# Kernel optimization log

Measured on AMD Instinct MI355X. Metric: run time of the kernel, lower is better.

## Reference

```python
import jax, jax.numpy as jnp
import numpy as np


def setup_inputs() -> dict:
    key = jax.random.key(0)
    k1, k2 = jax.random.split(key)
    B, C, H, W = 8, 16, 512, 512
    x = jax.random.normal(k1, (B, C, H, W), dtype=jnp.float32)
    # displacement field in voxel units, channels-first like the torch module
    phi = jax.random.normal(k2, (B, 2, H, W), dtype=jnp.float32) * 3.0
    return {"x": x, "phi": phi}


def _pull2d_wrap(img, disp):
    """img: [B,H,W,C], disp: [B,H,W,2] (displacement in voxels).
    Linear interpolation with circulant ('dft') boundary = wrap via mod."""
    B, H, W, C = img.shape
    gy = jnp.arange(H, dtype=img.dtype)[:, None]   # [H,1]
    gx = jnp.arange(W, dtype=img.dtype)[None, :]   # [1,W]
    cy = disp[..., 0] + gy                          # [B,H,W] sample coords (abs)
    cx = disp[..., 1] + gx
    y0f = jnp.floor(cy)
    x0f = jnp.floor(cx)
    wy = (cy - y0f)[..., None]                      # [B,H,W,1]
    wx = (cx - x0f)[..., None]
    y0 = jnp.mod(y0f.astype(jnp.int32), H)
    x0 = jnp.mod(x0f.astype(jnp.int32), W)
    y1 = jnp.mod(y0 + 1, H)
    x1 = jnp.mod(x0 + 1, W)

    def gather(im, yi, xi):                         # im [H,W,C]; yi,xi [H,W]
        return im[yi, xi]

    g = jax.vmap(gather)
    v00 = g(img, y0, x0)
    v01 = g(img, y0, x1)
    v10 = g(img, y1, x0)
    v11 = g(img, y1, x1)
    top = v00 * (1 - wx) + v01 * wx
    bot = v10 * (1 - wx) + v11 * wx
    return top * (1 - wy) + bot * wy                # [B,H,W,C]


def reference(x, phi):
    # x: [B,C,H,W], phi: [B,2,H,W] -> channels-last, pull, channels-first
    img = jnp.moveaxis(x, 1, -1)
    disp = jnp.moveaxis(phi, 1, -1)
    out = _pull2d_wrap(img, disp)
    return jnp.moveaxis(out, -1, 1)
```

## Files before the change

### kernel.cpp

```cpp
#include <hip/hip_runtime.h>


constexpr int B = 8, C = 16, H = 512, W = 512;
constexpr int HW = H * W;
constexpr int NXCD = 8;
constexpr int TPX = 1024;

typedef float    v4f __attribute__((ext_vector_type(4)));
typedef _Float16 v8h __attribute__((ext_vector_type(8)));

template <int CPX>
__device__ __forceinline__ int swz(int bid) {
    return (bid & (NXCD - 1)) * CPX + (bid >> 3);
}

__device__ __forceinline__ int lds_swz(int off) {
    return off ^ (((off >> 7) & 7) << 4);
}

__global__ __launch_bounds__(256) void transpose_lds_kernel(const float* __restrict__ x,
                                                            v8h* __restrict__ xt8) {
    __shared__ v8h lds[TPX * 2];
    constexpr int TCPX = (B * HW / TPX) / NXCD;
    int blk  = swz<TCPX>((int)blockIdx.x);
    int b    = blk >> 8;
    int tile = (blk & 255) * TPX;
    int t    = threadIdx.x;
    int px0  = t * 4;

    const float* xb = x + (size_t)b * C * HW + tile + px0;
    v8h r0[2], r1[2], r2[2], r3[2];
#pragma unroll
    for (int c = 0; c < 16; ++c) {
        v4f v = __builtin_nontemporal_load((const v4f*)(xb + (size_t)c * HW));
        int hh = c >> 3, j = c & 7;
        r0[hh][j] = (_Float16)v.x;
        r1[hh][j] = (_Float16)v.y;
        r2[hh][j] = (_Float16)v.z;
        r3[hh][j] = (_Float16)v.w;
    }

#pragma unroll
    for (int hh = 0; hh < 2; ++hh) {
        lds[lds_swz((px0 + 0) * 32 + hh * 16) >> 4] = r0[hh];
        lds[lds_swz((px0 + 1) * 32 + hh * 16) >> 4] = r1[hh];
        lds[lds_swz((px0 + 2) * 32 + hh * 16) >> 4] = r2[hh];
        lds[lds_swz((px0 + 3) * 32 + hh * 16) >> 4] = r3[hh];
    }
    __syncthreads();

    v8h* dst = xt8 + ((size_t)b * HW + tile) * 2;
#pragma unroll
    for (int s = 0; s < 8; ++s) {
        int off = s * 4096 + t * 16;
        dst[off >> 4] = lds[lds_swz(off) >> 4];
    }
}

__global__ __launch_bounds__(256) void gather_h_kernel(const v8h* __restrict__ xt8,
                                                       const float* __restrict__ phi,
                                                       float* __restrict__ out) {
    constexpr int CPX = (B * HW * 2 / 256) / NXCD;
    int idx = swz<CPX>((int)blockIdx.x) * 256 + (int)threadIdx.x;
    int b   = idx >> 19;
    int rem = idx & (HW * 2 - 1);
    int p   = rem >> 1;
    int q   = rem & 1;
    int h   = p >> 9;
    int w   = p & (W - 1);

    const float* phib = phi + (size_t)b * 2 * HW;
    float cy = __builtin_nontemporal_load(phib + p)      + (float)h;
    float cx = __builtin_nontemporal_load(phib + HW + p) + (float)w;

    float y0f = floorf(cy);
    float x0f = floorf(cx);
    float wy  = cy - y0f;
    float wx  = cx - x0f;

    int y0 = ((int)y0f) & (H - 1);
    int x0 = ((int)x0f) & (W - 1);
    int y1 = (y0 + 1)   & (H - 1);
    int x1 = (x0 + 1)   & (W - 1);

    const v8h* base = xt8 + (size_t)b * HW * 2;
    v8h v00 = base[(y0 * W + x0) * 2 + q];
    v8h v01 = base[(y0 * W + x1) * 2 + q];
    v8h v10 = base[(y1 * W + x0) * 2 + q];
    v8h v11 = base[(y1 * W + x1) * 2 + q];

    float omwx = 1.0f - wx;
    float omwy = 1.0f - wy;

    float* outp = out + ((size_t)b * C + q * 8) * HW + p;
#pragma unroll
    for (int j = 0; j < 8; ++j) {
        float top = (float)v00[j] * omwx + (float)v01[j] * wx;
        float bot = (float)v10[j] * omwx + (float)v11[j] * wx;
        __builtin_nontemporal_store(top * omwy + bot * wy, outp + (size_t)j * HW);
    }
}

__global__ __launch_bounds__(256) void pull_wrap_kernel(const float* __restrict__ x,
                                                        const float* __restrict__ phi,
                                                        float* __restrict__ out) {
    int idx = blockIdx.x * blockDim.x + threadIdx.x;
    if (idx >= B * HW) return;
    int b  = idx >> 18;
    int hw = idx & (HW - 1);
    int h  = hw >> 9;
    int w  = hw & (W - 1);

    const float* phib = phi + (size_t)b * 2 * HW;
    float cy = phib[hw]      + (float)h;
    float cx = phib[HW + hw] + (float)w;

    float y0f = floorf(cy);
    float x0f = floorf(cx);
    float wy  = cy - y0f;
    float wx  = cx - x0f;

    int y0 = ((int)y0f) & (H - 1);
    int x0 = ((int)x0f) & (W - 1);
    int y1 = (y0 + 1)   & (H - 1);
    int x1 = (x0 + 1)   & (W - 1);

    int o00 = y0 * W + x0;
    int o01 = y0 * W + x1;
    int o10 = y1 * W + x0;
    int o11 = y1 * W + x1;

    float omwx = 1.0f - wx;
    float omwy = 1.0f - wy;

    const float* plane = x   + (size_t)b * C * HW;
    float*       outp  = out + (size_t)b * C * HW + hw;

#pragma unroll
    for (int c = 0; c < C; ++c) {
        float v00 = plane[o00];
        float v01 = plane[o01];
        float v10 = plane[o10];
        float v11 = plane[o11];
        float top = v00 * omwx + v01 * wx;
        float bot = v10 * omwx + v11 * wx;
        outp[(size_t)c * HW] = top * omwy + bot * wy;
        plane += HW;
    }
}

extern "C" void kernel_launch(void* const* d_in, const int* in_sizes, int n_in,
                              void* d_out, int out_size, void* d_ws, size_t ws_size,
                              hipStream_t stream) {
    const float* x   = (const float*)d_in[0];
    const float* phi = (const float*)d_in[1];
    float* out = (float*)d_out;

    size_t need = (size_t)B * HW * C * sizeof(_Float16);
    if (d_ws != nullptr && ws_size >= need) {
        dim3 block(256);
        dim3 tgrid((B * HW) / TPX);
        dim3 ggrid((B * HW * 2) / 256);
        transpose_lds_kernel<<<tgrid, block, 0, stream>>>(x, (v8h*)d_ws);
        gather_h_kernel<<<ggrid, block, 0, stream>>>((const v8h*)d_ws, phi, out);
    } else {
        int n = B * HW;
        dim3 block(256);
        dim3 grid((n + 255) / 256);
        pull_wrap_kernel<<<grid, block, 0, stream>>>(x, phi, out);
    }
}
```

Measured before the change: 268.8 us.

## Split channel transpose and gather into two eight-channel passes

The fp16 channels-last transpose and bilinear gather now run as two passes of eight channels each, reusing a half-size workspace. Each gather thread handles one pixel and 8 channels instead of half a pixel pair. The intent is a smaller intermediate working set that stays resident in cache and a denser layout for the random gathers. In exchange there are two extra kernel launches and the displacement field is read twice.

New measurement: 276.4 us. 1.03x slower.

```diff
diff --git a/kernel.cpp b/kernel.cpp
--- a/kernel.cpp
+++ b/kernel.cpp
@@ -18,9 +18,10 @@
     return off ^ (((off >> 7) & 7) << 4);
 }
 
-__global__ __launch_bounds__(256) void transpose_lds_kernel(const float* __restrict__ x,
-                                                            v8h* __restrict__ xt8) {
-    __shared__ v8h lds[TPX * 2];
+__global__ __launch_bounds__(256) void transpose_oct_kernel(const float* __restrict__ x,
+                                                            v8h* __restrict__ xt,
+                                                            int h8) {
+    __shared__ v8h lds[TPX];
     constexpr int TCPX = (B * HW / TPX) / NXCD;
     int blk  = swz<TCPX>((int)blockIdx.x);
     int b    = blk >> 8;
@@ -28,44 +29,39 @@
     int t    = threadIdx.x;
     int px0  = t * 4;
 
-    const float* xb = x + (size_t)b * C * HW + tile + px0;
-    v8h r0[2], r1[2], r2[2], r3[2];
+    const float* xb = x + ((size_t)b * C + h8) * HW + tile + px0;
+    v8h r0, r1, r2, r3;
 #pragma unroll
-    for (int c = 0; c < 16; ++c) {
-        v4f v = __builtin_nontemporal_load((const v4f*)(xb + (size_t)c * HW));
-        int hh = c >> 3, j = c & 7;
-        r0[hh][j] = (_Float16)v.x;
-        r1[hh][j] = (_Float16)v.y;
-        r2[hh][j] = (_Float16)v.z;
-        r3[hh][j] = (_Float16)v.w;
+    for (int j = 0; j < 8; ++j) {
+        v4f v = __builtin_nontemporal_load((const v4f*)(xb + (size_t)j * HW));
+        r0[j] = (_Float16)v.x;
+        r1[j] = (_Float16)v.y;
+        r2[j] = (_Float16)v.z;
+        r3[j] = (_Float16)v.w;
     }
 
-#pragma unroll
-    for (int hh = 0; hh < 2; ++hh) {
-        lds[lds_swz((px0 + 0) * 32 + hh * 16) >> 4] = r0[hh];
-        lds[lds_swz((px0 + 1) * 32 + hh * 16) >> 4] = r1[hh];
-        lds[lds_swz((px0 + 2) * 32 + hh * 16) >> 4] = r2[hh];
-        lds[lds_swz((px0 + 3) * 32 + hh * 16) >> 4] = r3[hh];
-    }
+    lds[lds_swz((px0 + 0) * 16) >> 4] = r0;
+    lds[lds_swz((px0 + 1) * 16) >> 4] = r1;
+    lds[lds_swz((px0 + 2) * 16) >> 4] = r2;
+    lds[lds_swz((px0 + 3) * 16) >> 4] = r3;
     __syncthreads();
 
-    v8h* dst = xt8 + ((size_t)b * HW + tile) * 2;
+    v8h* dst = xt + (size_t)b * HW + tile;
 #pragma unroll
-    for (int s = 0; s < 8; ++s) {
+    for (int s = 0; s < 4; ++s) {
         int off = s * 4096 + t * 16;
         dst[off >> 4] = lds[lds_swz(off) >> 4];
     }
 }
 
-__global__ __launch_bounds__(256) void gather_h_kernel(const v8h* __restrict__ xt8,
-                                                       const float* __restrict__ phi,
-                                                       float* __restrict__ out) {
-    constexpr int CPX = (B * HW * 2 / 256) / NXCD;
+__global__ __launch_bounds__(256) void gather_oct_kernel(const v8h* __restrict__ xt,
+                                                         const float* __restrict__ phi,
+                                                         float* __restrict__ out,
+                                                         int h8) {
+    constexpr int CPX = (B * HW / 256) / NXCD;
     int idx = swz<CPX>((int)blockIdx.x) * 256 + (int)threadIdx.x;
-    int b   = idx >> 19;
-    int rem = idx & (HW * 2 - 1);
-    int p   = rem >> 1;
-    int q   = rem & 1;
+    int b   = idx >> 18;
+    int p   = idx & (HW - 1);
     int h   = p >> 9;
     int w   = p & (W - 1);
 
@@ -83,16 +79,16 @@
     int y1 = (y0 + 1)   & (H - 1);
     int x1 = (x0 + 1)   & (W - 1);
 
-    const v8h* base = xt8 + (size_t)b * HW * 2;
-    v8h v00 = base[(y0 * W + x0) * 2 + q];
-    v8h v01 = base[(y0 * W + x1) * 2 + q];
-    v8h v10 = base[(y1 * W + x0) * 2 + q];
-    v8h v11 = base[(y1 * W + x1) * 2 + q];
+    const v8h* base = xt + (size_t)b * HW;
+    v8h v00 = base[y0 * W + x0];
+    v8h v01 = base[y0 * W + x1];
+    v8h v10 = base[y1 * W + x0];
+    v8h v11 = base[y1 * W + x1];
 
     float omwx = 1.0f - wx;
     float omwy = 1.0f - wy;
 
-    float* outp = out + ((size_t)b * C + q * 8) * HW + p;
+    float* outp = out + ((size_t)b * C + h8) * HW + p;
 #pragma unroll
     for (int j = 0; j < 8; ++j) {
         float top = (float)v00[j] * omwx + (float)v01[j] * wx;
@@ -156,13 +152,15 @@
     const float* phi = (const float*)d_in[1];
     float* out = (float*)d_out;
 
-    size_t need = (size_t)B * HW * C * sizeof(_Float16);
+    size_t need = (size_t)B * HW * 8 * sizeof(_Float16);
     if (d_ws != nullptr && ws_size >= need) {
         dim3 block(256);
         dim3 tgrid((B * HW) / TPX);
-        dim3 ggrid((B * HW * 2) / 256);
-        transpose_lds_kernel<<<tgrid, block, 0, stream>>>(x, (v8h*)d_ws);
-        gather_h_kernel<<<ggrid, block, 0, stream>>>((const v8h*)d_ws, phi, out);
+        dim3 ggrid((B * HW) / 256);
+        transpose_oct_kernel<<<tgrid, block, 0, stream>>>(x, (v8h*)d_ws, 0);
+        gather_oct_kernel<<<ggrid, block, 0, stream>>>((const v8h*)d_ws, phi, out, 0);
+        transpose_oct_kernel<<<tgrid, block, 0, stream>>>(x, (v8h*)d_ws, 8);
+        gather_oct_kernel<<<ggrid, block, 0, stream>>>((const v8h*)d_ws, phi, out, 8);
     } else {
         int n = B * HW;
         dim3 block(256);
```
